# Kernel tuning notes

Measured on AMD Instinct MI355X. Metric: run time of the kernel, lower is better.

The kernel has to match this reference:

```python
import jax, jax.numpy as jnp
import numpy as np

VOCAB, FEAT, NCLS = 50000, 128, 20
N_NODES, N_EDGES = 50000, 1600000
H1, C1 = 8, 8  # conv1: 8 heads x 8 dims


def setup_inputs() -> dict:
    key = jax.random.key(0)
    ks = jax.random.split(key, 12)
    inp = {
        "x_ids": jax.random.randint(ks[0], (N_NODES,), 0, VOCAB),
        "edge_index": jax.random.randint(ks[1], (2, N_EDGES), 0, N_NODES),
        "emb": jax.random.normal(ks[2], (VOCAB, FEAT), jnp.float32) * 0.05,
        "W1": jax.random.normal(ks[3], (FEAT, H1 * C1), jnp.float32) * (1.0 / np.sqrt(FEAT)),
        "a_src1": jax.random.normal(ks[4], (H1, C1), jnp.float32) * 0.1,
        "a_dst1": jax.random.normal(ks[5], (H1, C1), jnp.float32) * 0.1,
        "b1": jnp.zeros((H1 * C1,), jnp.float32),
        "W2": jax.random.normal(ks[6], (H1 * C1, NCLS), jnp.float32) * (1.0 / np.sqrt(H1 * C1)),
        "a_src2": jax.random.normal(ks[7], (1, NCLS), jnp.float32) * 0.1,
        "a_dst2": jax.random.normal(ks[8], (1, NCLS), jnp.float32) * 0.1,
        "b2": jnp.zeros((NCLS,), jnp.float32),
    }
    return inp


def gat_conv(x, src, dst, W, a_src, a_dst, n_nodes):
    """One GATConv layer (PyG semantics, eval mode). Returns [N, H, C]."""
    H, C = a_src.shape
    xp = (x @ W).reshape(n_nodes, H, C)          # projected node feats
    asrc = jnp.sum(xp * a_src, axis=-1)          # [N, H]
    adst = jnp.sum(xp * a_dst, axis=-1)          # [N, H]
    e = jax.nn.leaky_relu(asrc[src] + adst[dst], negative_slope=0.2)  # [E, H]
    # segment softmax over incoming edges of each dst node (self-loops guarantee coverage)
    m = jax.ops.segment_max(e, dst, num_segments=n_nodes)
    p = jnp.exp(e - m[dst])
    s = jax.ops.segment_sum(p, dst, num_segments=n_nodes)
    alpha = p / s[dst]                           # [E, H]
    out = jax.ops.segment_sum(xp[src] * alpha[:, :, None], dst, num_segments=n_nodes)
    return out                                   # [N, H, C]


def reference(x_ids, edge_index, emb, W1, a_src1, a_dst1, b1, W2, a_src2, a_dst2, b2):
    n = x_ids.shape[0]
    loops = jnp.arange(n)
    src = jnp.concatenate([edge_index[0], loops])  # PyG GATConv adds self-loops
    dst = jnp.concatenate([edge_index[1], loops])

    x = emb[x_ids]                                  # embedding lookup, [N, FEAT]
    h = gat_conv(x, src, dst, W1, a_src1, a_dst1, n).reshape(n, -1) + b1  # concat heads
    h = jax.nn.elu(h)
    o = gat_conv(h, src, dst, W2, a_src2, a_dst2, n).mean(axis=1) + b2    # concat=False -> mean
    return jax.nn.log_softmax(o, axis=-1)
```

## Files before the change

### kernel.cpp

```cpp
#include <hip/hip_runtime.h>
#include <cstddef>


#define EPB 2048
#define NHB 256

typedef float f32x2 __attribute__((ext_vector_type(2)));

__device__ __forceinline__ float lrelu(float x) { return x > 0.f ? x : 0.2f * x; }
__device__ __forceinline__ int iadd(int* p, int v) {
  return __hip_atomic_fetch_add(p, v, __ATOMIC_RELAXED, __HIP_MEMORY_SCOPE_AGENT);
}
__device__ __forceinline__ unsigned f2bf(float f) {
  unsigned int u = __float_as_uint(f);
  u += 0x7FFFu + ((u >> 16) & 1u);
  return u >> 16;
}


__global__ __launch_bounds__(256) void k_bhist(
    const int* __restrict__ ei, int* __restrict__ bhistP, int E)
{
  __shared__ int h[256];
  h[threadIdx.x] = 0; __syncthreads();
  const int stride = NHB * 256;
  int e = blockIdx.x * 256 + threadIdx.x;
  for (; e + 3 * stride < E; e += 4 * stride) {
    int d0 = ei[E + e];
    int d1 = ei[E + e + stride];
    int d2 = ei[E + e + 2 * stride];
    int d3 = ei[E + e + 3 * stride];
    atomicAdd(&h[d0 >> 8], 1);
    atomicAdd(&h[d1 >> 8], 1);
    atomicAdd(&h[d2 >> 8], 1);
    atomicAdd(&h[d3 >> 8], 1);
  }
  for (; e < E; e += stride)
    atomicAdd(&h[ei[E + e] >> 8], 1);
  __syncthreads();
  bhistP[(blockIdx.x << 8) + threadIdx.x] = h[threadIdx.x];
}

__global__ __launch_bounds__(256) void k_bscan(
    const int* __restrict__ bhistP, int* __restrict__ bufOffs,
    int* __restrict__ tail, int nb)
{
  __shared__ int sp[256];
  const int tid = threadIdx.x;
  int v = 0;
#pragma unroll 8
  for (int b = 0; b < NHB; ++b) v += bhistP[(b << 8) + tid];
  sp[tid] = v; __syncthreads();
  for (int off = 1; off < 256; off <<= 1) {
    int t = (tid >= off) ? sp[tid - off] : 0;
    __syncthreads();
    sp[tid] += t;
    __syncthreads();
  }
  int excl = sp[tid] - v;
  if (tid < nb) { bufOffs[tid] = excl; tail[tid] = excl; }
  if (tid == 255) bufOffs[nb] = sp[255];
}

__global__ __launch_bounds__(256) void k_part(
    const int* __restrict__ ei, int* __restrict__ tail,
    int* __restrict__ buf, int E)
{
  __shared__ int sPair[EPB];
  __shared__ unsigned char sKey[EPB];
  __shared__ int sHist[256];
  __shared__ int sBase[256];
  const int tid = threadIdx.x;
  sHist[tid] = 0; __syncthreads();
  const int e0 = blockIdx.x * EPB;
  int m = E - e0; if (m > EPB) m = EPB;
  for (int i = tid; i < m; i += 256) {
    int d = __builtin_nontemporal_load(&ei[E + e0 + i]);
    int s = __builtin_nontemporal_load(&ei[e0 + i]);
    sPair[i] = ((d & 255) << 16) | s;
    int b = d >> 8;
    sKey[i] = (unsigned char)b;
    atomicAdd(&sHist[b], 1);
  }
  __syncthreads();
  int c = sHist[tid];
  sBase[tid] = c ? iadd(&tail[tid], c) : 0;
  sHist[tid] = 0;
  __syncthreads();
  for (int i = tid; i < m; i += 256) {
    int b = sKey[i];
    int off = atomicAdd(&sHist[b], 1);
    buf[sBase[b] + off] = sPair[i];
  }
}

__global__ __launch_bounds__(256) void k_coffs_scat(
    const int* __restrict__ buf, const int* __restrict__ bufOffs,
    int* __restrict__ offs, int* __restrict__ csr, int n)
{
  __shared__ int h[256];
  __shared__ int cur[256];
  const int b = blockIdx.x, tid = threadIdx.x;
  const int d = (b << 8) + tid;
  h[tid] = (d < n) ? 1 : 0;
  __syncthreads();
  const int lo = bufOffs[b], hi = bufOffs[b + 1];
  for (int i = lo + tid; i < hi; i += 256)
    atomicAdd(&h[(buf[i] >> 16) & 255], 1);
  __syncthreads();
  const int cnt = h[tid];
  for (int off = 1; off < 256; off <<= 1) {
    int t = (tid >= off) ? h[tid - off] : 0;
    __syncthreads();
    h[tid] += t;
    __syncthreads();
  }
  const int excl = h[tid] - cnt;
  const int base = lo + (b << 8);
  if (d < n) {
    const int o = base + excl;
    offs[d] = o;
    csr[o] = d << 6;
    cur[tid] = o + 1;
    if (d == n - 1) offs[n] = o + cnt;
  }
  __syncthreads();
  for (int i = lo + tid; i < hi; i += 256) {
    int p = buf[i];
    int pos = atomicAdd(&cur[(p >> 16) & 255], 1);
    csr[pos] = (p & 0xFFFF) << 6;
  }
}

__global__ __launch_bounds__(256) void k_embed_proj1(
    const int* __restrict__ x_ids, const float* __restrict__ emb,
    const float* __restrict__ W1, const float* __restrict__ a_dst1,
    unsigned char* __restrict__ xp1f8, float* __restrict__ adst1, int n)
{
  __shared__ float sWT[64 * 132];
  __shared__ float sx[4][2][128];
  for (int i = threadIdx.x; i < 128 * 64; i += 256) {
    int k = i >> 6, c = i & 63;
    sWT[c * 132 + k] = W1[i];
  }
  __syncthreads();
  const int wid = threadIdx.x >> 6;
  const int ln  = threadIdx.x & 63;
  const int ch  = ln;
  const int hh = ch >> 3, cc = ch & 7;
  const float ad = a_dst1[ch];
  const float* wrow = sWT + ch * 132;
  const int half = ln >> 5;
  const int qk   = ln & 31;
  float* myx = &sx[wid][0][0];
  float4 xv = make_float4(0.f, 0.f, 0.f, 0.f);
  {
    const int node_s = blockIdx.x * 32 + wid * 2 + half;
    if (node_s < n)
      xv = *(const float4*)(emb + (size_t)x_ids[node_s] * 128 + qk * 4);
  }
  for (int g = 0; g < 4; ++g) {
    *(float4*)(myx + half * 128 + qk * 4) = xv;
    float4 xnext = make_float4(0.f, 0.f, 0.f, 0.f);
    if (g < 3) {
      const int node_s = blockIdx.x * 32 + (g + 1) * 8 + wid * 2 + half;
      if (node_s < n)
        xnext = *(const float4*)(emb + (size_t)x_ids[node_s] * 128 + qk * 4);
    }
    asm volatile("s_waitcnt lgkmcnt(0)" ::: "memory");
    const int node0 = blockIdx.x * 32 + g * 8 + wid * 2;
    float acc0 = 0.f, acc1 = 0.f;
#pragma unroll 8
    for (int k = 0; k < 128; k += 4) {
      const float4 wv = *(const float4*)(wrow + k);
      const float4 x0 = *(const float4*)(myx + k);
      const float4 x1 = *(const float4*)(myx + 128 + k);
      acc0 = fmaf(x0.x, wv.x, acc0); acc1 = fmaf(x1.x, wv.x, acc1);
      acc0 = fmaf(x0.y, wv.y, acc0); acc1 = fmaf(x1.y, wv.y, acc1);
      acc0 = fmaf(x0.z, wv.z, acc0); acc1 = fmaf(x1.z, wv.z, acc1);
      acc0 = fmaf(x0.w, wv.w, acc0); acc1 = fmaf(x1.w, wv.w, acc1);
    }
    float vd0 = acc0 * ad, vd1 = acc1 * ad;
    vd0 += __shfl_xor(vd0, 1); vd0 += __shfl_xor(vd0, 2); vd0 += __shfl_xor(vd0, 4);
    vd1 += __shfl_xor(vd1, 1); vd1 += __shfl_xor(vd1, 2); vd1 += __shfl_xor(vd1, 4);
    const int node1 = node0 + 1;
    if (node0 < n) {
      unsigned int pk = (unsigned int)__builtin_amdgcn_cvt_pk_fp8_f32(
          acc0 * 16.f, acc0 * 16.f, 0, false);
      xp1f8[(size_t)node0 * 64 + ch] = (unsigned char)pk;
      if (cc == 0) adst1[node0 * 8 + hh] = vd0;
    }
    if (node1 < n) {
      unsigned int pk = (unsigned int)__builtin_amdgcn_cvt_pk_fp8_f32(
          acc1 * 16.f, acc1 * 16.f, 0, false);
      xp1f8[(size_t)node1 * 64 + ch] = (unsigned char)pk;
      if (cc == 0) adst1[node1 * 8 + hh] = vd1;
    }
    asm volatile("s_waitcnt lgkmcnt(0)" ::: "memory");
    xv = xnext;
  }
}

__global__ __launch_bounds__(256) void k_gather1(
    const int* __restrict__ offs, const int* __restrict__ csr,
    const float* __restrict__ a_src1, const float* __restrict__ adst1,
    const unsigned char* __restrict__ xp1f8,
    unsigned char* __restrict__ xp1h, int n)
{
  const int wid = threadIdx.x >> 6;
  const int ln  = threadIdx.x & 63;
  const int eslot = ln >> 3;
  const int h     = ln & 7;
  const int c0    = h << 3;
  const int d = blockIdx.x * 4 + wid;
  if (d >= n) return;
  const float4 a1lo0 = *(const float4*)(a_src1 + c0);
  const float4 a1hi0 = *(const float4*)(a_src1 + c0 + 4);
  const float s0 = a1lo0.x * 0.0625f, s1 = a1lo0.y * 0.0625f;
  const float s2 = a1lo0.z * 0.0625f, s3 = a1lo0.w * 0.0625f;
  const float s4 = a1hi0.x * 0.0625f, s5 = a1hi0.y * 0.0625f;
  const float s6 = a1hi0.z * 0.0625f, s7 = a1hi0.w * 0.0625f;
  const int beg = offs[d], end = offs[d + 1];
  const float adT = adst1[(size_t)d * 8 + h];
  const int hoff = h << 3;
  float a0=0.f,a1=0.f,a2=0.f,a3=0.f,a4=0.f,a5=0.f,a6=0.f,a7=0.f,den=0.f;
#pragma unroll 4
  for (int jb = beg + eslot; jb < end; jb += 8) {
    const int sv = __builtin_nontemporal_load(&csr[jb]);
    const uint2 u = *(const uint2*)(xp1f8 + (unsigned)sv + hoff);
    const f32x2 v01 = __builtin_amdgcn_cvt_pk_f32_fp8((int)u.x, false);
    const f32x2 v23 = __builtin_amdgcn_cvt_pk_f32_fp8((int)u.x, true);
    const f32x2 v45 = __builtin_amdgcn_cvt_pk_f32_fp8((int)u.y, false);
    const f32x2 v67 = __builtin_amdgcn_cvt_pk_f32_fp8((int)u.y, true);
    float dot = v01.x * s0;
    dot = fmaf(v01.y, s1, dot); dot = fmaf(v23.x, s2, dot);
    dot = fmaf(v23.y, s3, dot); dot = fmaf(v45.x, s4, dot);
    dot = fmaf(v45.y, s5, dot); dot = fmaf(v67.x, s6, dot);
    dot = fmaf(v67.y, s7, dot);
    const float p = __expf(lrelu(dot + adT));
    a0 = fmaf(p, v01.x, a0); a1 = fmaf(p, v01.y, a1);
    a2 = fmaf(p, v23.x, a2); a3 = fmaf(p, v23.y, a3);
    a4 = fmaf(p, v45.x, a4); a5 = fmaf(p, v45.y, a5);
    a6 = fmaf(p, v67.x, a6); a7 = fmaf(p, v67.y, a7);
    den += p;
  }
#pragma unroll
  for (int off = 8; off < 64; off <<= 1) {
    a0 += __shfl_xor(a0, off); a1 += __shfl_xor(a1, off);
    a2 += __shfl_xor(a2, off); a3 += __shfl_xor(a3, off);
    a4 += __shfl_xor(a4, off); a5 += __shfl_xor(a5, off);
    a6 += __shfl_xor(a6, off); a7 += __shfl_xor(a7, off);
    den += __shfl_xor(den, off);
  }
  if (eslot == 0) {
    const float inv16 = 1.f / den * 0.0625f;
    uint4 w;
    w.x = f2bf(a0 * inv16) | (f2bf(a1 * inv16) << 16);
    w.y = f2bf(a2 * inv16) | (f2bf(a3 * inv16) << 16);
    w.z = f2bf(a4 * inv16) | (f2bf(a5 * inv16) << 16);
    w.w = f2bf(a6 * inv16) | (f2bf(a7 * inv16) << 16);
    *(uint4*)(xp1h + (size_t)d * 128 + (h << 4)) = w;
  }
}

__global__ __launch_bounds__(256) void k_proj2(
    const unsigned char* __restrict__ xp1h, const float* __restrict__ b1,
    const float* __restrict__ W2, const float* __restrict__ a_src2,
    const float* __restrict__ a_dst2,
    unsigned int* __restrict__ xp2b, float* __restrict__ adst2, int n)
{
  __shared__ float sW[64 * 20];
  for (int i = threadIdx.x; i < 64 * 20; i += 256) sW[i] = W2[i];
  __syncthreads();
  const int node = blockIdx.x * 64 + (threadIdx.x >> 2);
  const int part = threadIdx.x & 3;
  if (node >= n) return;
  const int k0 = part * 16;
  const uint4 u0 = *(const uint4*)(xp1h + (size_t)node * 128 + k0 * 2);
  const uint4 u1 = *(const uint4*)(xp1h + (size_t)node * 128 + k0 * 2 + 16);
  float hv[16];
  {
    const unsigned uu[8] = {u0.x,u0.y,u0.z,u0.w,u1.x,u1.y,u1.z,u1.w};
#pragma unroll
    for (int j = 0; j < 8; ++j) {
      float t0 = __uint_as_float(uu[j] << 16)        + b1[k0 + 2*j];
      float t1 = __uint_as_float(uu[j] & 0xFFFF0000u) + b1[k0 + 2*j + 1];
      hv[2*j]   = t0 > 0.f ? t0 : expm1f(t0);
      hv[2*j+1] = t1 > 0.f ? t1 : expm1f(t1);
    }
  }
  float acc[20];
#pragma unroll
  for (int c = 0; c < 20; ++c) acc[c] = 0.f;
#pragma unroll
  for (int j = 0; j < 16; ++j) {
    const float hj = hv[j];
    const float* wr = sW + (k0 + j) * 20;
#pragma unroll
    for (int c = 0; c < 20; ++c) acc[c] = fmaf(hj, wr[c], acc[c]);
  }
#pragma unroll
  for (int c = 0; c < 20; ++c) {
    acc[c] += __shfl_xor(acc[c], 1);
    acc[c] += __shfl_xor(acc[c], 2);
  }
  float vs = 0.f, vd = 0.f;
#pragma unroll
  for (int c = 0; c < 20; ++c) {
    vs = fmaf(acc[c], a_src2[c], vs);
    vd = fmaf(acc[c], a_dst2[c], vd);
  }
  const int p5 = part * 5;
  uint4 w;
  w.x = f2bf(acc[p5 + 0]) | (f2bf(acc[p5 + 1]) << 16);
  w.y = f2bf(acc[p5 + 2]) | (f2bf(acc[p5 + 3]) << 16);
  w.z = f2bf(acc[p5 + 4]);
  w.w = __float_as_uint(vs);
  *(uint4*)(xp2b + (size_t)node * 16 + part * 4) = w;
  if (part == 0) adst2[node] = vd;
}

__global__ __launch_bounds__(256) void k_gather2(
    const int* __restrict__ offs, const int* __restrict__ csr,
    const float* __restrict__ adst2,
    const unsigned char* __restrict__ xp2c, const float* __restrict__ b2,
    float* __restrict__ out, int n)
{
  const int wid = threadIdx.x >> 6, ln = threadIdx.x & 63;
  const int eslot = ln >> 2, q = ln & 3;
  const int d = blockIdx.x * 4 + wid;
  if (d >= n) return;
  const int beg = offs[d], end = offs[d + 1];
  const float adT = adst2[d];
  const int qoff = q << 4;
  float a0=0.f,a1=0.f,a2=0.f,a3=0.f,a4=0.f,den=0.f;
#pragma unroll 2
  for (int jb = beg + eslot; jb < end; jb += 16) {
    const int sv = __builtin_nontemporal_load(&csr[jb]);
    const uint4 u = *(const uint4*)(xp2c + (unsigned)sv + qoff);
    const float p = __expf(lrelu(__uint_as_float(u.w) + adT));
    a0 = fmaf(p, __uint_as_float(u.x << 16), a0);
    a1 = fmaf(p, __uint_as_float(u.x & 0xFFFF0000u), a1);
    a2 = fmaf(p, __uint_as_float(u.y << 16), a2);
    a3 = fmaf(p, __uint_as_float(u.y & 0xFFFF0000u), a3);
    a4 = fmaf(p, __uint_as_float(u.z << 16), a4);
    den += p;
  }
#pragma unroll
  for (int off = 4; off < 64; off <<= 1) {
    a0 += __shfl_xor(a0, off); a1 += __shfl_xor(a1, off);
    a2 += __shfl_xor(a2, off); a3 += __shfl_xor(a3, off);
    a4 += __shfl_xor(a4, off);
    den += __shfl_xor(den, off);
  }
  const float inv = 1.f / den;
  const int c5 = q * 5;
  float o[5];
  float mx;
  {
    o[0] = a0 * inv + b2[c5 + 0];
    o[1] = a1 * inv + b2[c5 + 1];
    o[2] = a2 * inv + b2[c5 + 2];
    o[3] = a3 * inv + b2[c5 + 3];
    o[4] = a4 * inv + b2[c5 + 4];
    mx = fmaxf(fmaxf(fmaxf(o[0], o[1]), fmaxf(o[2], o[3])), o[4]);
  }
  mx = fmaxf(mx, __shfl_xor(mx, 1));
  mx = fmaxf(mx, __shfl_xor(mx, 2));
  float ss = __expf(o[0] - mx) + __expf(o[1] - mx) + __expf(o[2] - mx)
           + __expf(o[3] - mx) + __expf(o[4] - mx);
  ss += __shfl_xor(ss, 1);
  ss += __shfl_xor(ss, 2);
  const float lse = mx + __logf(ss);
  if (eslot == 0) {
#pragma unroll
    for (int j = 0; j < 5; ++j)
      out[(size_t)d * 20 + c5 + j] = o[j] - lse;
  }
}


extern "C" void kernel_launch(void* const* d_in, const int* in_sizes, int n_in,
                              void* d_out, int out_size, void* d_ws, size_t ws_size,
                              hipStream_t stream)
{
  const int*   x_ids  = (const int*)d_in[0];
  const int*   ei     = (const int*)d_in[1];
  const float* emb    = (const float*)d_in[2];
  const float* W1     = (const float*)d_in[3];
  const float* a_src1 = (const float*)d_in[4];
  const float* a_dst1 = (const float*)d_in[5];
  const float* b1     = (const float*)d_in[6];
  const float* W2     = (const float*)d_in[7];
  const float* a_src2 = (const float*)d_in[8];
  const float* a_dst2 = (const float*)d_in[9];
  const float* b2     = (const float*)d_in[10];
  float* out = (float*)d_out;

  const int n = in_sizes[0];
  const int E = in_sizes[1] / 2;
  const int nb = (n + 255) >> 8;

  char* base = (char*)d_ws;
  size_t r0 = (size_t)n * 64;
  if ((size_t)E * 4 > r0) r0 = (size_t)E * 4;
  r0 = (r0 + 255) & ~(size_t)255;
  unsigned char* xp1f8 = (unsigned char*)base;
  int*   buf   = (int*)base;
  float* adst1 = (float*)(base + r0);
  unsigned char* xp1h = (unsigned char*)(adst1 + (size_t)n * 8);
  unsigned int* xp2b = (unsigned int*)(xp1h + (size_t)n * 128);
  float* adst2 = (float*)(xp2b + (size_t)n * 16);
  int*   offs   = (int*)(adst2 + (size_t)n);
  int*   bhistP = offs + n + 1;
  int*   bufOffs= bhistP + NHB * 256;
  int*   tail   = bufOffs + 257;
  int*   csr    = tail + 256;

  k_bhist<<<NHB, 256, 0, stream>>>(ei, bhistP, E);
  k_bscan<<<1, 256, 0, stream>>>(bhistP, bufOffs, tail, nb);
  k_part<<<(E + EPB - 1) / EPB, 256, 0, stream>>>(ei, tail, buf, E);
  k_coffs_scat<<<nb, 256, 0, stream>>>(buf, bufOffs, offs, csr, n);

  k_embed_proj1<<<(n + 31) / 32, 256, 0, stream>>>(
      x_ids, emb, W1, a_dst1, xp1f8, adst1, n);

  k_gather1<<<(n + 3) / 4, 256, 0, stream>>>(
      offs, csr, a_src1, adst1, xp1f8, xp1h, n);

  k_proj2<<<(n + 63) / 64, 256, 0, stream>>>(
      xp1h, b1, W2, a_src2, a_dst2, xp2b, adst2, n);

  k_gather2<<<(n + 3) / 4, 256, 0, stream>>>(
      offs, csr, adst2, (const unsigned char*)xp2b, b2, out, n);
}
```

Measured before the change: 187.6 us.

## Merge CSR finalize and embedding projection into one heterogeneous launch

Fuses the CSR offset/scatter kernel and the embedding+layer-1 projection kernel into a single launch, with block indices below nb doing CSR work and the rest doing projection. This removes a kernel launch boundary and lets the two independent stages run concurrently on the GPU. Because xp1f8 previously aliased the partition buffer, it is moved to a separate workspace region after csr. The cost is a larger workspace footprint and a shared memory allocation sized for the larger role in every block, which may reduce occupancy for the CSR blocks.

```diff
diff --git a/kernel.cpp b/kernel.cpp
--- a/kernel.cpp
+++ b/kernel.cpp
@@ -94,51 +94,52 @@
   }
 }
 
-__global__ __launch_bounds__(256) void k_coffs_scat(
+__global__ __launch_bounds__(256) void k_coffs_embed(
     const int* __restrict__ buf, const int* __restrict__ bufOffs,
-    int* __restrict__ offs, int* __restrict__ csr, int n)
-{
-  __shared__ int h[256];
-  __shared__ int cur[256];
-  const int b = blockIdx.x, tid = threadIdx.x;
-  const int d = (b << 8) + tid;
-  h[tid] = (d < n) ? 1 : 0;
-  __syncthreads();
-  const int lo = bufOffs[b], hi = bufOffs[b + 1];
-  for (int i = lo + tid; i < hi; i += 256)
-    atomicAdd(&h[(buf[i] >> 16) & 255], 1);
-  __syncthreads();
-  const int cnt = h[tid];
-  for (int off = 1; off < 256; off <<= 1) {
-    int t = (tid >= off) ? h[tid - off] : 0;
-    __syncthreads();
-    h[tid] += t;
-    __syncthreads();
-  }
-  const int excl = h[tid] - cnt;
-  const int base = lo + (b << 8);
-  if (d < n) {
-    const int o = base + excl;
-    offs[d] = o;
-    csr[o] = d << 6;
-    cur[tid] = o + 1;
-    if (d == n - 1) offs[n] = o + cnt;
-  }
-  __syncthreads();
-  for (int i = lo + tid; i < hi; i += 256) {
-    int p = buf[i];
-    int pos = atomicAdd(&cur[(p >> 16) & 255], 1);
-    csr[pos] = (p & 0xFFFF) << 6;
-  }
-}
-
-__global__ __launch_bounds__(256) void k_embed_proj1(
+    int* __restrict__ offs, int* __restrict__ csr, int nb,
     const int* __restrict__ x_ids, const float* __restrict__ emb,
     const float* __restrict__ W1, const float* __restrict__ a_dst1,
     unsigned char* __restrict__ xp1f8, float* __restrict__ adst1, int n)
 {
-  __shared__ float sWT[64 * 132];
-  __shared__ float sx[4][2][128];
+  __shared__ __align__(16) char smem[37888];
+  if ((int)blockIdx.x < nb) {
+    int* h   = (int*)smem;
+    int* cur = h + 256;
+    const int b = blockIdx.x, tid = threadIdx.x;
+    const int d = (b << 8) + tid;
+    h[tid] = (d < n) ? 1 : 0;
+    __syncthreads();
+    const int lo = bufOffs[b], hi = bufOffs[b + 1];
+    for (int i = lo + tid; i < hi; i += 256)
+      atomicAdd(&h[(buf[i] >> 16) & 255], 1);
+    __syncthreads();
+    const int cnt = h[tid];
+    for (int off = 1; off < 256; off <<= 1) {
+      int t = (tid >= off) ? h[tid - off] : 0;
+      __syncthreads();
+      h[tid] += t;
+      __syncthreads();
+    }
+    const int excl = h[tid] - cnt;
+    const int base = lo + (b << 8);
+    if (d < n) {
+      const int o = base + excl;
+      offs[d] = o;
+      csr[o] = d << 6;
+      cur[tid] = o + 1;
+      if (d == n - 1) offs[n] = o + cnt;
+    }
+    __syncthreads();
+    for (int i = lo + tid; i < hi; i += 256) {
+      int p = buf[i];
+      int pos = atomicAdd(&cur[(p >> 16) & 255], 1);
+      csr[pos] = (p & 0xFFFF) << 6;
+    }
+    return;
+  }
+  float* sWT = (float*)smem;
+  float* sxb = sWT + 64 * 132;
+  const int eb = blockIdx.x - nb;
   for (int i = threadIdx.x; i < 128 * 64; i += 256) {
     int k = i >> 6, c = i & 63;
     sWT[c * 132 + k] = W1[i];
@@ -152,10 +153,10 @@
   const float* wrow = sWT + ch * 132;
   const int half = ln >> 5;
   const int qk   = ln & 31;
-  float* myx = &sx[wid][0][0];
+  float* myx = sxb + wid * 256;
   float4 xv = make_float4(0.f, 0.f, 0.f, 0.f);
   {
-    const int node_s = blockIdx.x * 32 + wid * 2 + half;
+    const int node_s = eb * 32 + wid * 2 + half;
     if (node_s < n)
       xv = *(const float4*)(emb + (size_t)x_ids[node_s] * 128 + qk * 4);
   }
@@ -163,12 +164,12 @@
     *(float4*)(myx + half * 128 + qk * 4) = xv;
     float4 xnext = make_float4(0.f, 0.f, 0.f, 0.f);
     if (g < 3) {
-      const int node_s = blockIdx.x * 32 + (g + 1) * 8 + wid * 2 + half;
+      const int node_s = eb * 32 + (g + 1) * 8 + wid * 2 + half;
       if (node_s < n)
         xnext = *(const float4*)(emb + (size_t)x_ids[node_s] * 128 + qk * 4);
     }
     asm volatile("s_waitcnt lgkmcnt(0)" ::: "memory");
-    const int node0 = blockIdx.x * 32 + g * 8 + wid * 2;
+    const int node0 = eb * 32 + g * 8 + wid * 2;
     float acc0 = 0.f, acc1 = 0.f;
 #pragma unroll 8
     for (int k = 0; k < 128; k += 4) {
@@ -417,13 +418,19 @@
   int*   tail   = bufOffs + 257;
   int*   csr    = tail + 256;
 
+  unsigned char* xp1f8_real = (unsigned char*)(csr + (size_t)E + n);
+  xp1f8 = xp1f8_real;
+
   k_bhist<<<NHB, 256, 0, stream>>>(ei, bhistP, E);
   k_bscan<<<1, 256, 0, stream>>>(bhistP, bufOffs, tail, nb);
   k_part<<<(E + EPB - 1) / EPB, 256, 0, stream>>>(ei, tail, buf, E);
-  k_coffs_scat<<<nb, 256, 0, stream>>>(buf, bufOffs, offs, csr, n);
-
-  k_embed_proj1<<<(n + 31) / 32, 256, 0, stream>>>(
-      x_ids, emb, W1, a_dst1, xp1f8, adst1, n);
+
+  {
+    const int embBlocks = (n + 31) / 32;
+    k_coffs_embed<<<nb + embBlocks, 256, 0, stream>>>(
+        buf, bufOffs, offs, csr, nb,
+        x_ids, emb, W1, a_dst1, xp1f8, adst1, n);
+  }
 
   k_gather1<<<(n + 3) / 4, 256, 0, stream>>>(
       offs, csr, a_src1, adst1, xp1f8, xp1h, n);
```

After: 166.6 us. -11.2%, faster.
